# Kernel optimization log

Measured on AMD Instinct MI355X. Metric: run time of the kernel, lower is better.

## Reference

```python
import jax, jax.numpy as jnp
import numpy as np

D_MODEL = 1024
NUM_HEADS = 16
MODULUS = 2147483647
B, S = 2, 2048


def setup_inputs() -> dict:
    key = jax.random.key(0)
    d = D_MODEL
    names_dims = [
        ('q_w', d, d), ('k_w', d, d), ('v_w', d, d), ('o_w', d, d),
        ('emb1_w', 1, d // 2), ('emb2_w', d // 2, d),
        ('log_w', 1, d // 4), ('prime_w', 10, d // 4),
        ('div_w', 20, d // 4), ('bit_w', 32, d // 4),
        ('fus_w', d, d),
    ]
    ks = jax.random.split(key, len(names_dims) + 3)
    inp = {}
    for (name, fin, fout), k in zip(names_dims, ks[:len(names_dims)]):
        inp[name] = jax.random.normal(k, (fin, fout), jnp.float32) * 0.02
        inp[name.replace('_w', '_b')] = jnp.zeros((fout,), jnp.float32)
    inp['arith_bias'] = jax.random.normal(ks[-3], (NUM_HEADS, 1, 1), jnp.float32)
    inp['gcd_weight'] = jnp.ones((1,), jnp.float32)
    inp['encodings'] = jax.random.randint(ks[-2], (B, S), 1, 1000000, dtype=jnp.int32)
    return inp


def reference(encodings, q_w, q_b, k_w, k_b, v_w, v_b, o_w, o_b,
              emb1_w, emb1_b, emb2_w, emb2_b, log_w, log_b,
              prime_w, prime_b, div_w, div_b, bit_w, bit_b,
              fus_w, fus_b, arith_bias, gcd_weight):
    Bz, Sz = encodings.shape
    d = q_w.shape[0]
    H = NUM_HEADS
    hd = d // H

    # --- ArithmeticEmbedding ---
    ef = encodings.astype(jnp.float32)
    norm = (ef / MODULUS)[..., None]                       # [B,S,1]
    base = jnp.maximum(norm @ emb1_w + emb1_b, 0.0) @ emb2_w + emb2_b
    logf = jnp.log(ef + 1.0)[..., None] @ log_w + log_b    # [B,S,d/4]
    primes = jnp.array([2, 3, 5, 7, 11, 13, 17, 19, 23, 29], dtype=jnp.int32)
    pf = (encodings[..., None] % primes == 0).astype(jnp.float32) @ prime_w + prime_b
    tv = jnp.arange(2, 22, dtype=jnp.int32)
    df = ((encodings[..., None] % tv).astype(jnp.float32) / tv.astype(jnp.float32)) @ div_w + div_b
    shifts = jnp.arange(32, dtype=jnp.int32)
    bf = (((encodings[..., None] >> shifts) & 1)).astype(jnp.float32) @ bit_w + bit_b
    feats = jnp.concatenate([logf, pf, df, bf], axis=-1)   # [B,S,d]
    hidden = base + feats @ fus_w + fus_b

    # --- ArithmeticAttention ---
    q = (hidden @ q_w + q_b).reshape(Bz, Sz, H, hd)
    k = (hidden @ k_w + k_b).reshape(Bz, Sz, H, hd)
    v = (hidden @ v_w + v_b).reshape(Bz, Sz, H, hd)
    scores = jnp.einsum('bihd,bjhd->bhij', q, k) / jnp.sqrt(jnp.float32(hd))
    # vectorized arithmetic bias (original is an O(S^2) python loop)
    ei = encodings[:, :, None]
    ej = encodings[:, None, :]
    gcd_approx = jnp.minimum(ei % (ej + 1), ej % (ei + 1)).astype(jnp.float32)
    bias = gcd_approx / (jnp.maximum(ei, ej) + 1).astype(jnp.float32)
    bias = jnp.where(jnp.eye(Sz, dtype=bool)[None], 0.0, bias)  # i==j -> 0
    scores = scores + bias[:, None] * gcd_weight + arith_bias
    attn = jax.nn.softmax(scores, axis=-1)
    out = jnp.einsum('bhij,bjhd->bihd', attn, v).reshape(Bz, Sz, d)
    return out @ o_w + o_b
```

## Files before the change

### kernel.cpp

```cpp
#include <hip/hip_runtime.h>
#include <hip/hip_bf16.h>

typedef unsigned short u16;
typedef __attribute__((ext_vector_type(8))) __bf16 bf16x8;
typedef __attribute__((ext_vector_type(4))) float f32x4;
typedef __attribute__((ext_vector_type(16))) float f32x16;

#define SEQ 2048
#define NB 2
#define NH 16
#define HD 64
#define DM 1024
#define LDQKV 3072
#define KF 576
#define LOG2E 1.4426950408889634f
#define NSPL 3

__device__ __forceinline__ u16 f2bf(float f) {
    unsigned u = __float_as_uint(f);
    unsigned r = u + 0x7FFFu + ((u >> 16) & 1u);
    return (u16)(r >> 16);
}
__device__ __forceinline__ float bf2f(u16 x) {
    return __uint_as_float(((unsigned)x) << 16);
}
__device__ __forceinline__ unsigned cvt_pk_bf16(float a, float b) {
    unsigned r;
    asm("v_cvt_pk_bf16_f32 %0, %1, %2" : "=v"(r) : "v"(a), "v"(b));
    return r;
}
__device__ __forceinline__ void gl_lds16(const u16* g, u16* l) {
    __builtin_amdgcn_global_load_lds((const __attribute__((address_space(1))) unsigned int*)g,
                                     (__attribute__((address_space(3))) unsigned int*)l, 16, 0, 0);
}
__device__ __forceinline__ unsigned fmod_u24(unsigned a, unsigned b) {
    float q = truncf(__fdividef((float)a, (float)b));
    int r = (int)a - (int)((unsigned)q * b);
    r += (r < 0) ? (int)b : 0;
    r -= (r >= (int)b) ? (int)b : 0;
    return (unsigned)r;
}

__global__ __launch_bounds__(256) void transw4_kernel(const float* __restrict__ q_w,
                                                      const float* __restrict__ k_w,
                                                      const float* __restrict__ v_w,
                                                      const float* __restrict__ o_w,
                                                      u16* __restrict__ WqkvT,
                                                      u16* __restrict__ WoT) {
    __shared__ float tl[32][33];
    const int z = blockIdx.z;
    const float* src = (z == 0) ? q_w : (z == 1) ? k_w : (z == 2) ? v_w : o_w;
    u16* dst = (z < 3) ? WqkvT + (size_t)z * 1024 * DM : WoT;
    const float scale = (z == 0) ? 0.125f * LOG2E : 1.0f;
    int tx = threadIdx.x, ty = threadIdx.y;
    int n = blockIdx.x * 32 + tx;
    int kbase = blockIdx.y * 32;
#pragma unroll
    for (int i = 0; i < 4; ++i)
        tl[ty + i * 8][tx] = src[(size_t)(kbase + ty + i * 8) * DM + n];
    __syncthreads();
    int k = kbase + tx;
#pragma unroll
    for (int i = 0; i < 4; ++i) {
        int n2 = blockIdx.x * 32 + ty + i * 8;
        dst[(size_t)n2 * DM + k] = f2bf(tl[tx][ty + i * 8] * scale);
    }
}

__global__ __launch_bounds__(256) void castwc_kernel(const float* __restrict__ src,
                                                     u16* __restrict__ Wc) {
    int i = (blockIdx.x * 256 + threadIdx.x) * 4;
    float4 v = *(const float4*)&src[i];
    uint2 o;
    o.x = cvt_pk_bf16(v.x, v.y);
    o.y = cvt_pk_bf16(v.z, v.w);
    *(uint2*)&Wc[i] = o;
}

__global__ void cvec_kernel(const float* __restrict__ emb2_b, const float* __restrict__ fus_b,
                            const float* __restrict__ log_b, const float* __restrict__ prime_b,
                            const float* __restrict__ div_b, const float* __restrict__ bit_b,
                            const float* __restrict__ fus_w, float* __restrict__ cvec) {
    int n = blockIdx.x * 256 + threadIdx.x;
    float acc = emb2_b[n] + fus_b[n];
#pragma unroll 4
    for (int m = 0; m < 256; ++m) {
        acc += log_b[m]   * fus_w[(size_t)m * DM + n];
        acc += prime_b[m] * fus_w[(size_t)(256 + m) * DM + n];
        acc += div_b[m]   * fus_w[(size_t)(512 + m) * DM + n];
        acc += bit_b[m]   * fus_w[(size_t)(768 + m) * DM + n];
    }
    cvec[n] = acc;
}

__global__ __launch_bounds__(256) void fold_kernel(const float* __restrict__ log_w,
                                                   const float* __restrict__ prime_w,
                                                   const float* __restrict__ div_w,
                                                   const float* __restrict__ bit_w,
                                                   const float* __restrict__ fus_w,
                                                   const float* __restrict__ cvec,
                                                   u16* __restrict__ Wc) {
    const int r = blockIdx.y;
    const int n = blockIdx.x * 256 + threadIdx.x;
    if (r == 63) { Wc[(size_t)575 * DM + n] = f2bf(cvec[n]); return; }
    const float* wrow; int chunk;
    if (r == 0)       { wrow = log_w;                 chunk = 0;   }
    else if (r < 11)  { wrow = prime_w + (r - 1) * 256; chunk = 256; }
    else if (r < 31)  { wrow = div_w + (r - 11) * 256;  chunk = 512; }
    else              { wrow = bit_w + (r - 31) * 256;  chunk = 768; }
    float acc = 0.f;
#pragma unroll 8
    for (int m = 0; m < 256; ++m)
        acc += wrow[m] * fus_w[(size_t)(chunk + m) * DM + n];
    Wc[(size_t)(512 + r) * DM + n] = f2bf(acc);
}

__global__ void qkvb_kernel(const float* __restrict__ q_b, const float* __restrict__ k_b,
                            const float* __restrict__ v_b, float* __restrict__ qkvb) {
    int i = blockIdx.x * 256 + threadIdx.x;
    const float C1 = 0.125f * LOG2E;
    qkvb[i] = (i < 1024) ? q_b[i] * C1 : (i < 2048 ? k_b[i - 1024] : v_b[i - 2048]);
}

__global__ __launch_bounds__(256) void feat_kernel(const int* __restrict__ enc,
                                                   const float* __restrict__ emb1_w,
                                                   const float* __restrict__ emb1_b,
                                                   u16* __restrict__ F) {
    const int tok = blockIdx.x;
    const int t = threadIdx.x;
    int e = enc[tok];
    float ef = (float)e;
    float nrm = ef / 2147483647.0f;
    for (int k = t; k < 512; k += 256)
        F[(size_t)tok * KF + k] = f2bf(fmaxf(nrm * emb1_w[k] + emb1_b[k], 0.f));
    if (t < 64) {
        float v;
        if (t == 0) v = logf(ef + 1.f);
        else if (t < 11) {
            const int pr[10] = {2, 3, 5, 7, 11, 13, 17, 19, 23, 29};
            v = (e % pr[t - 1] == 0) ? 1.f : 0.f;
        } else if (t < 31) {
            int tv = t - 11 + 2;
            v = (float)(e % tv) / (float)tv;
        } else if (t < 63) {
            int sh = t - 31;
            v = (float)((e >> sh) & 1);
        } else v = 1.0f;
        F[(size_t)tok * KF + 512 + t] = f2bf(v);
    }
}

template <int OUT_BF16, int TN, int HB>
__global__ __launch_bounds__(256) void gemm_kernel(const u16* __restrict__ A,
                                                   const u16* __restrict__ BT,
                                                   const float* __restrict__ bias,
                                                   void* __restrict__ Cv,
                                                   int M, int N, int K) {
    constexpr int FN = TN / 32;
    __shared__ u16 As[128 * 32];
    __shared__ u16 Bs[TN * 32];
    const int t = threadIdx.x;
    const int w = t >> 6, l = t & 63, lr = l & 15, lg = l >> 4;
    const int m0 = blockIdx.y * 128, n0 = blockIdx.x * TN;
    const int wm = (w >> 1) * 64, wn = (w & 1) * (TN / 2);
    const int srow = l >> 2, scol = (l & 3) * 8;

    const u16* gA = &A[(size_t)(m0 + w * 32 + srow) * K + scol];
    u16* lA = &As[w * 1024];
    const u16* gB;
    u16* lB;
    if (TN == 128) { gB = &BT[(size_t)(n0 + w * 32 + srow) * K + scol]; lB = &Bs[w * 1024]; }
    else           { gB = &BT[(size_t)(n0 + w * 16 + srow) * K + scol]; lB = &Bs[w * 512];  }

    f32x4 acc[4][FN] = {};
    for (int k0 = 0; k0 < K; k0 += 32) {
        __syncthreads();
        gl_lds16(gA + k0, lA);
        gl_lds16(gA + k0 + (size_t)16 * K, lA + 512);
        if (TN == 128) {
            gl_lds16(gB + k0, lB);
            gl_lds16(gB + k0 + (size_t)16 * K, lB + 512);
        } else {
            gl_lds16(gB + k0, lB);
        }
        __syncthreads();
        bf16x8 a[4], b[FN];
#pragma unroll
        for (int i = 0; i < 4; ++i) a[i] = *(const bf16x8*)&As[(wm + i * 16 + lr) * 32 + lg * 8];
#pragma unroll
        for (int j = 0; j < FN; ++j) b[j] = *(const bf16x8*)&Bs[(wn + j * 16 + lr) * 32 + lg * 8];
#pragma unroll
        for (int mi = 0; mi < 4; ++mi)
#pragma unroll
            for (int ni = 0; ni < FN; ++ni)
                acc[mi][ni] = __builtin_amdgcn_mfma_f32_16x16x32_bf16(a[mi], b[ni], acc[mi][ni], 0, 0, 0);
    }
#pragma unroll
    for (int mi = 0; mi < 4; ++mi)
#pragma unroll
        for (int ni = 0; ni < FN; ++ni)
#pragma unroll
            for (int r = 0; r < 4; ++r) {
                int row = m0 + wm + mi * 16 + lg * 4 + r;
                int col = n0 + wn + ni * 16 + lr;
                float v = acc[mi][ni][r] + (HB ? bias[col] : 0.f);
                if (OUT_BF16)
                    ((u16*)Cv)[(size_t)row * N + col] = f2bf(v);
                else
                    ((float*)Cv)[(size_t)row * N + col] = v;
            }
}

__global__ __launch_bounds__(256) void vtrans_kernel(const u16* __restrict__ qkv,
                                                     u16* __restrict__ vT) {
    __shared__ u16 tile[64][72];
    int t = threadIdx.x;
    int s0 = blockIdx.x * 64, h = blockIdx.y, b = blockIdx.z;
    int sr = t >> 2, sc = (t & 3) * 16;
    const int4* g = (const int4*)&qkv[(size_t)(b * SEQ + s0 + sr) * LDQKV + 2048 + h * HD + sc];
    int4 v0 = g[0], v1 = g[1];
    *(int4*)&tile[sr][sc] = v0;
    *(int4*)&tile[sr][sc + 8] = v1;
    __syncthreads();
    int dl = sr, j0 = sc;
    u16 tmp[16];
#pragma unroll
    for (int jj = 0; jj < 16; ++jj) tmp[jj] = tile[j0 + jj][dl];
    u16* out = &vT[(size_t)((b * NH + h) * HD + dl) * SEQ + s0 + j0];
    *(int4*)&out[0] = *(int4*)&tmp[0];
    *(int4*)&out[8] = *(int4*)&tmp[8];
}

__global__ __launch_bounds__(256) void biasm_kernel(const int* __restrict__ enc,
                                                    const float* __restrict__ gcd_w,
                                                    float* __restrict__ bias2) {
    int vi = blockIdx.x * 256 + threadIdx.x;
    int i  = vi & 2047;
    int rr = (vi >> 11) & 15;
    int jt = (vi >> 15) & 31;
    int b  = vi >> 20;
    int j0 = jt * 64 + rr * 4;
    unsigned ei = (unsigned)enc[b * SEQ + i];
    float scale = gcd_w[0] * LOG2E;
    f32x4 o;
#pragma unroll
    for (int e = 0; e < 4; ++e) {
        int j = j0 + e;
        unsigned ej = (unsigned)enc[b * SEQ + j];
        unsigned r1 = fmod_u24(ei, ej + 1u);
        unsigned r2 = fmod_u24(ej, ei + 1u);
        float g = (float)min(r1, r2);
        float mx = (float)(max(ei, ej) + 1u);
        o[e] = (i == j) ? 0.f : __fdividef(g, mx) * scale;
    }
    *(f32x4*)&bias2[(size_t)vi * 4] = o;
}

#define KVB 64
#define SWZ(row, cb) ((((int)(row)) << 7) + (((int)(cb)) ^ ((((int)(row)) & 7) << 4)))

__global__ __launch_bounds__(256, 3) void attn_kernel(const u16* __restrict__ qkv,
                                                      const u16* __restrict__ vT,
                                                      const float* __restrict__ bias2,
                                                      u16* __restrict__ Opart,
                                                      float* __restrict__ Lp,
                                                      float* __restrict__ Mp) {
    __shared__ char smem[49152];
    const int t = threadIdx.x, w = t >> 6, l = t & 63;
    const int q5 = l & 31, hi = l >> 5;
    char* PlB = smem + 32768 + (w << 12);
    const int qt = blockIdx.x, h = blockIdx.y;
    const int b = blockIdx.z / NSPL, sp = blockIdx.z % NSPL;
    const int qrow = qt * 128 + w * 32 + q5;
    const int jt0 = sp * 11;
    const int NT  = (sp == 2) ? 10 : 11;
    const int j0s = jt0 * KVB;

    bf16x8 qf[4];
#pragma unroll
    for (int ks = 0; ks < 4; ++ks)
        qf[ks] = *(const bf16x8*)&qkv[(size_t)(b * SEQ + qrow) * LDQKV + h * HD + ks * 16 + hi * 8];

    const int sr = t >> 2, sc = (t & 3) * 16;
    const u16* gK = &qkv[(size_t)(b * SEQ + j0s + sr) * LDQKV + 1024 + h * HD + sc];
    const u16* gV = &vT[(size_t)((b * NH + h) * HD + sr) * SEQ + j0s + sc];
    const float* gBl = &bias2[((((size_t)b * 32 + jt0) * 16 + hi) * 2048 + qrow) * 4];

    int4 kr0 = *(const int4*)&gK[0], kr1 = *(const int4*)&gK[8];
    int4 vr0 = *(const int4*)&gV[0], vr1 = *(const int4*)&gV[8];
    f32x4 br[8];
#pragma unroll
    for (int c = 0; c < 2; ++c)
#pragma unroll
        for (int g = 0; g < 4; ++g)
            br[c * 4 + g] = *(const f32x4*)&gBl[(size_t)(8 * c + 2 * g) << 13];

    float m_s = -1e30f, l_s = 0.f;
    f32x16 acc2[2] = {};

    for (int lt = 0; lt < NT; ++lt) {
        char* KtB = smem + (lt & 1) * 16384;
        char* VtB = KtB + 8192;
        *(int4*)(KtB + SWZ(sr, (t & 3) * 32))      = kr0;
        *(int4*)(KtB + SWZ(sr, (t & 3) * 32 + 16)) = kr1;
        *(int4*)(VtB + SWZ(sr, (t & 3) * 32))      = vr0;
        *(int4*)(VtB + SWZ(sr, (t & 3) * 32 + 16)) = vr1;
        if (lt < NT - 1) {
            kr0 = *(const int4*)&gK[(size_t)(lt + 1) * KVB * LDQKV];
            kr1 = *(const int4*)&gK[(size_t)(lt + 1) * KVB * LDQKV + 8];
            vr0 = *(const int4*)&gV[(lt + 1) * KVB];
            vr1 = *(const int4*)&gV[(lt + 1) * KVB + 8];
        }
        __syncthreads();

        f32x16 s2[2];
#pragma unroll
        for (int c = 0; c < 2; ++c)
#pragma unroll
            for (int g = 0; g < 4; ++g)
#pragma unroll
                for (int e = 0; e < 4; ++e)
                    s2[c][g * 4 + e] = br[c * 4 + g][e];
        if (lt < NT - 1) {
            const float* nB = gBl + ((size_t)(lt + 1) << 17);
#pragma unroll
            for (int c = 0; c < 2; ++c)
#pragma unroll
                for (int g = 0; g < 4; ++g)
                    br[c * 4 + g] = *(const f32x4*)&nB[(size_t)(8 * c + 2 * g) << 13];
        }

        __builtin_amdgcn_s_setprio(1);
#pragma unroll
        for (int ks = 0; ks < 4; ++ks)
#pragma unroll
            for (int c = 0; c < 2; ++c) {
                bf16x8 kf = *(const bf16x8*)(KtB + SWZ(32 * c + q5, ks * 32 + hi * 16));
                s2[c] = __builtin_amdgcn_mfma_f32_32x32x16_bf16(kf, qf[ks], s2[c], 0, 0, 0);
            }
        __builtin_amdgcn_s_setprio(0);

        float tm = s2[0][0];
#pragma unroll
        for (int c = 0; c < 2; ++c)
#pragma unroll
            for (int r = 0; r < 16; ++r) tm = fmaxf(tm, s2[c][r]);
        tm = fmaxf(tm, __shfl_xor(tm, 32));

        if (__any(tm > m_s + 8.f)) {
            float mn = fmaxf(m_s, tm);
            float al = __builtin_exp2f(m_s - mn);
            l_s *= al;
            m_s = mn;
#pragma unroll
            for (int dc = 0; dc < 2; ++dc)
#pragma unroll
                for (int r = 0; r < 16; ++r) acc2[dc][r] *= al;
        }

        float ps = 0.f;
#pragma unroll
        for (int c = 0; c < 2; ++c)
#pragma unroll
            for (int r = 0; r < 16; ++r) {
                float p = __builtin_exp2f(s2[c][r] - m_s);
                s2[c][r] = p;
                ps += p;
            }
        ps += __shfl_xor(ps, 32);
        l_s += ps;

#pragma unroll
        for (int c = 0; c < 2; ++c)
#pragma unroll
            for (int g = 0; g < 4; ++g) {
                uint2 u;
                u.x = cvt_pk_bf16(s2[c][4 * g + 0], s2[c][4 * g + 1]);
                u.y = cvt_pk_bf16(s2[c][4 * g + 2], s2[c][4 * g + 3]);
                *(uint2*)(PlB + SWZ(q5, (32 * c + 8 * g + 4 * hi) * 2)) = u;
            }
        asm volatile("s_waitcnt lgkmcnt(0)" ::: "memory");
        __builtin_amdgcn_sched_barrier(0);

        __builtin_amdgcn_s_setprio(1);
#pragma unroll
        for (int ks = 0; ks < 4; ++ks) {
            bf16x8 pb = *(const bf16x8*)(PlB + SWZ(q5, ks * 32 + hi * 16));
#pragma unroll
            for (int dc = 0; dc < 2; ++dc) {
                bf16x8 vf = *(const bf16x8*)(VtB + SWZ(32 * dc + q5, ks * 32 + hi * 16));
                acc2[dc] = __builtin_amdgcn_mfma_f32_32x32x16_bf16(vf, pb, acc2[dc], 0, 0, 0);
            }
        }
        __builtin_amdgcn_s_setprio(0);
    }

    u16* orow = &Opart[(size_t)((sp * NB + b) * SEQ + qrow) * DM + h * HD];
#pragma unroll
    for (int dc = 0; dc < 2; ++dc)
#pragma unroll
        for (int g = 0; g < 4; ++g) {
            uint2 u;
            u.x = cvt_pk_bf16(acc2[dc][4 * g + 0], acc2[dc][4 * g + 1]);
            u.y = cvt_pk_bf16(acc2[dc][4 * g + 2], acc2[dc][4 * g + 3]);
            *(uint2*)&orow[32 * dc + 8 * g + 4 * hi] = u;
        }
    if (hi == 0) {
        size_t idx = ((size_t)(sp * NB + b) * SEQ + qrow) * NH + h;
        Lp[idx] = l_s;
        Mp[idx] = m_s;
    }
}

__global__ __launch_bounds__(256) void comb_kernel(const u16* __restrict__ Opart,
                                                   const float* __restrict__ Lp,
                                                   const float* __restrict__ Mp,
                                                   u16* __restrict__ attn_o) {
    int tid = blockIdx.x * 256 + threadIdx.x;
    int base = tid * 4;
    int b = base / (SEQ * DM);
    int rem = base - b * SEQ * DM;
    int i = rem / DM;
    int c = rem - i * DM;
    int h = c >> 6;
    size_t ix[3];
    float m[3], lv[3];
#pragma unroll
    for (int s = 0; s < 3; ++s) {
        ix[s] = ((size_t)(s * NB + b) * SEQ + i) * NH + h;
        m[s] = Mp[ix[s]];
        lv[s] = Lp[ix[s]];
    }
    float ms = fmaxf(fmaxf(m[0], m[1]), m[2]);
    float a0 = __builtin_exp2f(m[0] - ms);
    float a1 = __builtin_exp2f(m[1] - ms);
    float a2 = __builtin_exp2f(m[2] - ms);
    float inv = 1.f / (a0 * lv[0] + a1 * lv[1] + a2 * lv[2]);
    a0 *= inv; a1 *= inv; a2 *= inv;
    uint2 o0 = *(const uint2*)&Opart[((size_t)(0 * NB + b) * SEQ + i) * DM + c];
    uint2 o1 = *(const uint2*)&Opart[((size_t)(1 * NB + b) * SEQ + i) * DM + c];
    uint2 o2 = *(const uint2*)&Opart[((size_t)(2 * NB + b) * SEQ + i) * DM + c];
    float v0 = a0 * bf2f(o0.x & 0xFFFF) + a1 * bf2f(o1.x & 0xFFFF) + a2 * bf2f(o2.x & 0xFFFF);
    float v1 = a0 * bf2f(o0.x >> 16)    + a1 * bf2f(o1.x >> 16)    + a2 * bf2f(o2.x >> 16);
    float v2 = a0 * bf2f(o0.y & 0xFFFF) + a1 * bf2f(o1.y & 0xFFFF) + a2 * bf2f(o2.y & 0xFFFF);
    float v3 = a0 * bf2f(o0.y >> 16)    + a1 * bf2f(o1.y >> 16)    + a2 * bf2f(o2.y >> 16);
    uint2 u;
    u.x = cvt_pk_bf16(v0, v1);
    u.y = cvt_pk_bf16(v2, v3);
    *(uint2*)&attn_o[(size_t)(b * SEQ + i) * DM + c] = u;
}

extern "C" void kernel_launch(void* const* d_in, const int* in_sizes, int n_in,
                              void* d_out, int out_size, void* d_ws, size_t ws_size,
                              hipStream_t stream) {
    const float* q_w    = (const float*)d_in[0];
    const float* q_b    = (const float*)d_in[1];
    const float* k_w    = (const float*)d_in[2];
    const float* k_b    = (const float*)d_in[3];
    const float* v_w    = (const float*)d_in[4];
    const float* v_b    = (const float*)d_in[5];
    const float* o_w    = (const float*)d_in[6];
    const float* o_b    = (const float*)d_in[7];
    const float* emb1_w = (const float*)d_in[8];
    const float* emb1_b = (const float*)d_in[9];
    const float* emb2_w = (const float*)d_in[10];
    const float* emb2_b = (const float*)d_in[11];
    const float* log_w  = (const float*)d_in[12];
    const float* log_b  = (const float*)d_in[13];
    const float* prime_w= (const float*)d_in[14];
    const float* prime_b= (const float*)d_in[15];
    const float* div_w  = (const float*)d_in[16];
    const float* div_b  = (const float*)d_in[17];
    const float* bit_w  = (const float*)d_in[18];
    const float* bit_b  = (const float*)d_in[19];
    const float* fus_w  = (const float*)d_in[20];
    const float* fus_b  = (const float*)d_in[21];
    const float* gcd_weight = (const float*)d_in[23];
    const int*   enc    = (const int*)d_in[24];

    char* ws = (char*)d_ws;
    size_t off = 0;
    auto alloc = [&](size_t bytes) {
        char* p = ws + off;
        off += (bytes + 255) & ~size_t(255);
        return p;
    };
    u16*   WqkvT  = (u16*)alloc((size_t)3072 * DM * 2);
    u16*   WoT    = (u16*)alloc((size_t)DM * DM * 2);
    u16*   Wc     = (u16*)alloc((size_t)KF * DM * 2);
    u16*   W2T    = (u16*)alloc((size_t)3072 * KF * 2);
    float* cvec   = (float*)alloc(DM * 4);
    float* qkvb   = (float*)alloc(3072 * 4);
    u16*   F      = (u16*)alloc((size_t)NB * SEQ * KF * 2);
    u16*   qkv    = (u16*)alloc((size_t)NB * SEQ * LDQKV * 2);
    u16*   vT     = (u16*)alloc((size_t)NB * NH * HD * SEQ * 2);
    float* bias2  = (float*)alloc((size_t)NB * SEQ * SEQ * 4);
    u16*   attn_o = (u16*)alloc((size_t)NB * SEQ * DM * 2);
    u16*   Opart  = (u16*)alloc((size_t)NSPL * NB * SEQ * DM * 2);
    float* Lp     = (float*)alloc((size_t)NSPL * NB * SEQ * NH * 4);
    float* Mp     = (float*)alloc((size_t)NSPL * NB * SEQ * NH * 4);
    (void)ws_size; (void)n_in; (void)in_sizes; (void)out_size;

    transw4_kernel<<<dim3(32, 32, 4), dim3(32, 8), 0, stream>>>(q_w, k_w, v_w, o_w, WqkvT, WoT);
    castwc_kernel<<<512, 256, 0, stream>>>(emb2_w, Wc);
    cvec_kernel<<<4, 256, 0, stream>>>(emb2_b, fus_b, log_b, prime_b, div_b, bit_b, fus_w, cvec);
    fold_kernel<<<dim3(4, 64), 256, 0, stream>>>(log_w, prime_w, div_w, bit_w, fus_w, cvec, Wc);
    qkvb_kernel<<<12, 256, 0, stream>>>(q_b, k_b, v_b, qkvb);

    gemm_kernel<1, 64, 0><<<dim3(KF / 64, 3072 / 128), 256, 0, stream>>>(WqkvT, Wc, nullptr, W2T,
                                                                         3072, KF, DM);
    feat_kernel<<<NB * SEQ, 256, 0, stream>>>(enc, emb1_w, emb1_b, F);
    gemm_kernel<1, 128, 1><<<dim3(3072 / 128, NB * SEQ / 128), 256, 0, stream>>>(F, W2T, qkvb, qkv,
                                                                                 NB * SEQ, 3072, KF);
    vtrans_kernel<<<dim3(SEQ / 64, NH, NB), 256, 0, stream>>>(qkv, vT);
    biasm_kernel<<<NB * 32 * 16 * SEQ / 256, 256, 0, stream>>>(enc, gcd_weight, bias2);
    attn_kernel<<<dim3(SEQ / 128, NH, NB * NSPL), 256, 0, stream>>>(qkv, vT, bias2, Opart, Lp, Mp);
    comb_kernel<<<NB * SEQ * DM / 4 / 256, 256, 0, stream>>>(Opart, Lp, Mp, attn_o);
    gemm_kernel<0, 64, 1><<<dim3(DM / 64, NB * SEQ / 128), 256, 0, stream>>>(attn_o, WoT, o_b, d_out,
                                                                             NB * SEQ, DM, DM);
}
```

Before: 225.3 us.

## Merge prep kernels and feed bias tile directly as MFMA accumulator

Several small setup kernels (weight cast, cvec, qkv bias, features, bias matrix) are folded into fewer launches: the emb2 cast joins the transpose kernel, cvec moves into fold_kernel, and the bias, feature and qkv-bias work are combined into one prep kernel. The arithmetic bias is rewritten in an MFMA-accumulator-native layout so the attention kernel loads it as two 16-float vectors and passes it as the initial accumulator of the first QK MFMA, removing the per-element register shuffle. This cuts launch overhead and attention register moves, at the cost of a more intricate index mapping that must match the MFMA output layout exactly.

```diff
diff --git a/kernel.cpp b/kernel.cpp
--- a/kernel.cpp
+++ b/kernel.cpp
@@ -41,18 +41,31 @@
     return (unsigned)r;
 }
 
-__global__ __launch_bounds__(256) void transw4_kernel(const float* __restrict__ q_w,
+__global__ __launch_bounds__(256) void transw5_kernel(const float* __restrict__ q_w,
                                                       const float* __restrict__ k_w,
                                                       const float* __restrict__ v_w,
                                                       const float* __restrict__ o_w,
+                                                      const float* __restrict__ emb2_w,
                                                       u16* __restrict__ WqkvT,
-                                                      u16* __restrict__ WoT) {
+                                                      u16* __restrict__ WoT,
+                                                      u16* __restrict__ Wc) {
+    const int z = blockIdx.z;
+    int tx = threadIdx.x, ty = threadIdx.y;
+    if (z >= 4) {
+        int blin = blockIdx.y * 32 + blockIdx.x;
+        if (blin >= 512) return;
+        int i = (blin * 256 + ty * 32 + tx) * 4;
+        float4 v = *(const float4*)&emb2_w[i];
+        uint2 o;
+        o.x = cvt_pk_bf16(v.x, v.y);
+        o.y = cvt_pk_bf16(v.z, v.w);
+        *(uint2*)&Wc[i] = o;
+        return;
+    }
     __shared__ float tl[32][33];
-    const int z = blockIdx.z;
     const float* src = (z == 0) ? q_w : (z == 1) ? k_w : (z == 2) ? v_w : o_w;
     u16* dst = (z < 3) ? WqkvT + (size_t)z * 1024 * DM : WoT;
     const float scale = (z == 0) ? 0.125f * LOG2E : 1.0f;
-    int tx = threadIdx.x, ty = threadIdx.y;
     int n = blockIdx.x * 32 + tx;
     int kbase = blockIdx.y * 32;
 #pragma unroll
@@ -65,32 +78,6 @@
         int n2 = blockIdx.x * 32 + ty + i * 8;
         dst[(size_t)n2 * DM + k] = f2bf(tl[tx][ty + i * 8] * scale);
     }
-}
-
-__global__ __launch_bounds__(256) void castwc_kernel(const float* __restrict__ src,
-                                                     u16* __restrict__ Wc) {
-    int i = (blockIdx.x * 256 + threadIdx.x) * 4;
-    float4 v = *(const float4*)&src[i];
-    uint2 o;
-    o.x = cvt_pk_bf16(v.x, v.y);
-    o.y = cvt_pk_bf16(v.z, v.w);
-    *(uint2*)&Wc[i] = o;
-}
-
-__global__ void cvec_kernel(const float* __restrict__ emb2_b, const float* __restrict__ fus_b,
-                            const float* __restrict__ log_b, const float* __restrict__ prime_b,
-                            const float* __restrict__ div_b, const float* __restrict__ bit_b,
-                            const float* __restrict__ fus_w, float* __restrict__ cvec) {
-    int n = blockIdx.x * 256 + threadIdx.x;
-    float acc = emb2_b[n] + fus_b[n];
-#pragma unroll 4
-    for (int m = 0; m < 256; ++m) {
-        acc += log_b[m]   * fus_w[(size_t)m * DM + n];
-        acc += prime_b[m] * fus_w[(size_t)(256 + m) * DM + n];
-        acc += div_b[m]   * fus_w[(size_t)(512 + m) * DM + n];
-        acc += bit_b[m]   * fus_w[(size_t)(768 + m) * DM + n];
-    }
-    cvec[n] = acc;
 }
 
 __global__ __launch_bounds__(256) void fold_kernel(const float* __restrict__ log_w,
@@ -98,11 +85,27 @@
                                                    const float* __restrict__ div_w,
                                                    const float* __restrict__ bit_w,
                                                    const float* __restrict__ fus_w,
-                                                   const float* __restrict__ cvec,
+                                                   const float* __restrict__ emb2_b,
+                                                   const float* __restrict__ fus_b,
+                                                   const float* __restrict__ log_b,
+                                                   const float* __restrict__ prime_b,
+                                                   const float* __restrict__ div_b,
+                                                   const float* __restrict__ bit_b,
                                                    u16* __restrict__ Wc) {
     const int r = blockIdx.y;
     const int n = blockIdx.x * 256 + threadIdx.x;
-    if (r == 63) { Wc[(size_t)575 * DM + n] = f2bf(cvec[n]); return; }
+    if (r == 63) {
+        float acc = emb2_b[n] + fus_b[n];
+#pragma unroll 4
+        for (int m = 0; m < 256; ++m) {
+            acc += log_b[m]   * fus_w[(size_t)m * DM + n];
+            acc += prime_b[m] * fus_w[(size_t)(256 + m) * DM + n];
+            acc += div_b[m]   * fus_w[(size_t)(512 + m) * DM + n];
+            acc += bit_b[m]   * fus_w[(size_t)(768 + m) * DM + n];
+        }
+        Wc[(size_t)575 * DM + n] = f2bf(acc);
+        return;
+    }
     const float* wrow; int chunk;
     if (r == 0)       { wrow = log_w;                 chunk = 0;   }
     else if (r < 11)  { wrow = prime_w + (r - 1) * 256; chunk = 256; }
@@ -115,38 +118,62 @@
     Wc[(size_t)(512 + r) * DM + n] = f2bf(acc);
 }
 
-__global__ void qkvb_kernel(const float* __restrict__ q_b, const float* __restrict__ k_b,
-                            const float* __restrict__ v_b, float* __restrict__ qkvb) {
-    int i = blockIdx.x * 256 + threadIdx.x;
-    const float C1 = 0.125f * LOG2E;
-    qkvb[i] = (i < 1024) ? q_b[i] * C1 : (i < 2048 ? k_b[i - 1024] : v_b[i - 2048]);
-}
-
-__global__ __launch_bounds__(256) void feat_kernel(const int* __restrict__ enc,
+__global__ __launch_bounds__(256) void prep_kernel(const int* __restrict__ enc,
+                                                   const float* __restrict__ gcd_w,
                                                    const float* __restrict__ emb1_w,
                                                    const float* __restrict__ emb1_b,
-                                                   u16* __restrict__ F) {
-    const int tok = blockIdx.x;
-    const int t = threadIdx.x;
-    int e = enc[tok];
-    float ef = (float)e;
-    float nrm = ef / 2147483647.0f;
-    for (int k = t; k < 512; k += 256)
-        F[(size_t)tok * KF + k] = f2bf(fmaxf(nrm * emb1_w[k] + emb1_b[k], 0.f));
-    if (t < 64) {
-        float v;
-        if (t == 0) v = logf(ef + 1.f);
-        else if (t < 11) {
-            const int pr[10] = {2, 3, 5, 7, 11, 13, 17, 19, 23, 29};
-            v = (e % pr[t - 1] == 0) ? 1.f : 0.f;
-        } else if (t < 31) {
-            int tv = t - 11 + 2;
-            v = (float)(e % tv) / (float)tv;
-        } else if (t < 63) {
-            int sh = t - 31;
-            v = (float)((e >> sh) & 1);
-        } else v = 1.0f;
-        F[(size_t)tok * KF + 512 + t] = f2bf(v);
+                                                   const float* __restrict__ q_b,
+                                                   const float* __restrict__ k_b,
+                                                   const float* __restrict__ v_b,
+                                                   float* __restrict__ bias3,
+                                                   u16* __restrict__ F,
+                                                   float* __restrict__ qkvb) {
+    const int bx = blockIdx.x, t = threadIdx.x;
+    if (bx < 8192) {
+        int tid = bx * 256 + t;
+        int g = tid & 3, hi = (tid >> 2) & 1, i = (tid >> 3) & 2047, tile2 = tid >> 14;
+        int c = tile2 & 1, jt = (tile2 >> 1) & 31, b = tile2 >> 6;
+        unsigned ei = (unsigned)enc[b * SEQ + i];
+        float scale = gcd_w[0] * LOG2E;
+        int j0 = jt * 64 + 32 * c + 8 * g + 4 * hi;
+        int4 ej4 = *(const int4*)&enc[b * SEQ + j0];
+        f32x4 o;
+#pragma unroll
+        for (int e = 0; e < 4; ++e) {
+            unsigned ej = (unsigned)((e == 0) ? ej4.x : (e == 1) ? ej4.y : (e == 2) ? ej4.z : ej4.w);
+            unsigned r1 = fmod_u24(ei, ej + 1u);
+            unsigned r2 = fmod_u24(ej, ei + 1u);
+            float gg = (float)min(r1, r2);
+            float mx = (float)(max(ei, ej) + 1u);
+            o[e] = (i == j0 + e) ? 0.f : __fdividef(gg, mx) * scale;
+        }
+        *(f32x4*)&bias3[(size_t)tid * 4] = o;
+    } else if (bx < 12288) {
+        const int tok = bx - 8192;
+        int e = enc[tok];
+        float ef = (float)e;
+        float nrm = ef / 2147483647.0f;
+        for (int k = t; k < 512; k += 256)
+            F[(size_t)tok * KF + k] = f2bf(fmaxf(nrm * emb1_w[k] + emb1_b[k], 0.f));
+        if (t < 64) {
+            float v;
+            if (t == 0) v = logf(ef + 1.f);
+            else if (t < 11) {
+                const int pr[10] = {2, 3, 5, 7, 11, 13, 17, 19, 23, 29};
+                v = (e % pr[t - 1] == 0) ? 1.f : 0.f;
+            } else if (t < 31) {
+                int tv = t - 11 + 2;
+                v = (float)(e % tv) / (float)tv;
+            } else if (t < 63) {
+                int sh = t - 31;
+                v = (float)((e >> sh) & 1);
+            } else v = 1.0f;
+            F[(size_t)tok * KF + 512 + t] = f2bf(v);
+        }
+    } else {
+        int i = (bx - 12288) * 256 + t;
+        const float C1 = 0.125f * LOG2E;
+        qkvb[i] = (i < 1024) ? q_b[i] * C1 : (i < 2048 ? k_b[i - 1024] : v_b[i - 2048]);
     }
 }
 
@@ -231,37 +258,12 @@
     *(int4*)&out[8] = *(int4*)&tmp[8];
 }
 
-__global__ __launch_bounds__(256) void biasm_kernel(const int* __restrict__ enc,
-                                                    const float* __restrict__ gcd_w,
-                                                    float* __restrict__ bias2) {
-    int vi = blockIdx.x * 256 + threadIdx.x;
-    int i  = vi & 2047;
-    int rr = (vi >> 11) & 15;
-    int jt = (vi >> 15) & 31;
-    int b  = vi >> 20;
-    int j0 = jt * 64 + rr * 4;
-    unsigned ei = (unsigned)enc[b * SEQ + i];
-    float scale = gcd_w[0] * LOG2E;
-    f32x4 o;
-#pragma unroll
-    for (int e = 0; e < 4; ++e) {
-        int j = j0 + e;
-        unsigned ej = (unsigned)enc[b * SEQ + j];
-        unsigned r1 = fmod_u24(ei, ej + 1u);
-        unsigned r2 = fmod_u24(ej, ei + 1u);
-        float g = (float)min(r1, r2);
-        float mx = (float)(max(ei, ej) + 1u);
-        o[e] = (i == j) ? 0.f : __fdividef(g, mx) * scale;
-    }
-    *(f32x4*)&bias2[(size_t)vi * 4] = o;
-}
-
 #define KVB 64
 #define SWZ(row, cb) ((((int)(row)) << 7) + (((int)(cb)) ^ ((((int)(row)) & 7) << 4)))
 
 __global__ __launch_bounds__(256, 3) void attn_kernel(const u16* __restrict__ qkv,
                                                       const u16* __restrict__ vT,
-                                                      const float* __restrict__ bias2,
+                                                      const float* __restrict__ bias3,
                                                       u16* __restrict__ Opart,
                                                       float* __restrict__ Lp,
                                                       float* __restrict__ Mp) {
@@ -284,16 +286,13 @@
     const int sr = t >> 2, sc = (t & 3) * 16;
     const u16* gK = &qkv[(size_t)(b * SEQ + j0s + sr) * LDQKV + 1024 + h * HD + sc];
     const u16* gV = &vT[(size_t)((b * NH + h) * HD + sr) * SEQ + j0s + sc];
-    const float* gBl = &bias2[((((size_t)b * 32 + jt0) * 16 + hi) * 2048 + qrow) * 4];
+    const float* gB3 = &bias3[((((size_t)(b * 32 + jt0) * 2) * 2048 + qrow) * 2 + hi) * 16];
 
     int4 kr0 = *(const int4*)&gK[0], kr1 = *(const int4*)&gK[8];
     int4 vr0 = *(const int4*)&gV[0], vr1 = *(const int4*)&gV[8];
-    f32x4 br[8];
-#pragma unroll
-    for (int c = 0; c < 2; ++c)
-#pragma unroll
-        for (int g = 0; g < 4; ++g)
-            br[c * 4 + g] = *(const f32x4*)&gBl[(size_t)(8 * c + 2 * g) << 13];
+    f32x16 brv[2];
+    brv[0] = *(const f32x16*)(gB3);
+    brv[1] = *(const f32x16*)(gB3 + 65536);
 
     float m_s = -1e30f, l_s = 0.f;
     f32x16 acc2[2] = {};
@@ -314,25 +313,22 @@
         __syncthreads();
 
         f32x16 s2[2];
-#pragma unroll
-        for (int c = 0; c < 2; ++c)
-#pragma unroll
-            for (int g = 0; g < 4; ++g)
-#pragma unroll
-                for (int e = 0; e < 4; ++e)
-                    s2[c][g * 4 + e] = br[c * 4 + g][e];
+        __builtin_amdgcn_s_setprio(1);
+        {
+            bf16x8 kf0 = *(const bf16x8*)(KtB + SWZ(q5, hi * 16));
+            s2[0] = __builtin_amdgcn_mfma_f32_32x32x16_bf16(kf0, qf[0], brv[0], 0, 0, 0);
+            bf16x8 kf1 = *(const bf16x8*)(KtB + SWZ(32 + q5, hi * 16));
+            s2[1] = __builtin_amdgcn_mfma_f32_32x32x16_bf16(kf1, qf[0], brv[1], 0, 0, 0);
+        }
+        __builtin_amdgcn_s_setprio(0);
         if (lt < NT - 1) {
-            const float* nB = gBl + ((size_t)(lt + 1) << 17);
-#pragma unroll
-            for (int c = 0; c < 2; ++c)
-#pragma unroll
-                for (int g = 0; g < 4; ++g)
-                    br[c * 4 + g] = *(const f32x4*)&nB[(size_t)(8 * c + 2 * g) << 13];
-        }
-
+            const float* nB = gB3 + (size_t)(lt + 1) * 131072;
+            brv[0] = *(const f32x16*)(nB);
+            brv[1] = *(const f32x16*)(nB + 65536);
+        }
         __builtin_amdgcn_s_setprio(1);
 #pragma unroll
-        for (int ks = 0; ks < 4; ++ks)
+        for (int ks = 1; ks < 4; ++ks)
 #pragma unroll
             for (int c = 0; c < 2; ++c) {
                 bf16x8 kf = *(const bf16x8*)(KtB + SWZ(32 * c + q5, ks * 32 + hi * 16));
@@ -489,32 +485,29 @@
     u16*   WoT    = (u16*)alloc((size_t)DM * DM * 2);
     u16*   Wc     = (u16*)alloc((size_t)KF * DM * 2);
     u16*   W2T    = (u16*)alloc((size_t)3072 * KF * 2);
-    float* cvec   = (float*)alloc(DM * 4);
     float* qkvb   = (float*)alloc(3072 * 4);
     u16*   F      = (u16*)alloc((size_t)NB * SEQ * KF * 2);
     u16*   qkv    = (u16*)alloc((size_t)NB * SEQ * LDQKV * 2);
     u16*   vT     = (u16*)alloc((size_t)NB * NH * HD * SEQ * 2);
-    float* bias2  = (float*)alloc((size_t)NB * SEQ * SEQ * 4);
+    float* bias3  = (float*)alloc((size_t)NB * SEQ * SEQ * 4);
     u16*   attn_o = (u16*)alloc((size_t)NB * SEQ * DM * 2);
     u16*   Opart  = (u16*)alloc((size_t)NSPL * NB * SEQ * DM * 2);
     float* Lp     = (float*)alloc((size_t)NSPL * NB * SEQ * NH * 4);
     float* Mp     = (float*)alloc((size_t)NSPL * NB * SEQ * NH * 4);
     (void)ws_size; (void)n_in; (void)in_sizes; (void)out_size;
 
-    transw4_kernel<<<dim3(32, 32, 4), dim3(32, 8), 0, stream>>>(q_w, k_w, v_w, o_w, WqkvT, WoT);
-    castwc_kernel<<<512, 256, 0, stream>>>(emb2_w, Wc);
-    cvec_kernel<<<4, 256, 0, stream>>>(emb2_b, fus_b, log_b, prime_b, div_b, bit_b, fus_w, cvec);
-    fold_kernel<<<dim3(4, 64), 256, 0, stream>>>(log_w, prime_w, div_w, bit_w, fus_w, cvec, Wc);
-    qkvb_kernel<<<12, 256, 0, stream>>>(q_b, k_b, v_b, qkvb);
-
+    transw5_kernel<<<dim3(32, 32, 5), dim3(32, 8), 0, stream>>>(q_w, k_w, v_w, o_w, emb2_w,
+                                                                WqkvT, WoT, Wc);
+    fold_kernel<<<dim3(4, 64), 256, 0, stream>>>(log_w, prime_w, div_w, bit_w, fus_w,
+                                                 emb2_b, fus_b, log_b, prime_b, div_b, bit_b, Wc);
+    prep_kernel<<<12300, 256, 0, stream>>>(enc, gcd_weight, emb1_w, emb1_b, q_b, k_b, v_b,
+                                           bias3, F, qkvb);
     gemm_kernel<1, 64, 0><<<dim3(KF / 64, 3072 / 128), 256, 0, stream>>>(WqkvT, Wc, nullptr, W2T,
                                                                          3072, KF, DM);
-    feat_kernel<<<NB * SEQ, 256, 0, stream>>>(enc, emb1_w, emb1_b, F);
     gemm_kernel<1, 128, 1><<<dim3(3072 / 128, NB * SEQ / 128), 256, 0, stream>>>(F, W2T, qkvb, qkv,
                                                                                  NB * SEQ, 3072, KF);
     vtrans_kernel<<<dim3(SEQ / 64, NH, NB), 256, 0, stream>>>(qkv, vT);
-    biasm_kernel<<<NB * 32 * 16 * SEQ / 256, 256, 0, stream>>>(enc, gcd_weight, bias2);
-    attn_kernel<<<dim3(SEQ / 128, NH, NB * NSPL), 256, 0, stream>>>(qkv, vT, bias2, Opart, Lp, Mp);
+    attn_kernel<<<dim3(SEQ / 128, NH, NB * NSPL), 256, 0, stream>>>(qkv, vT, bias3, Opart, Lp, Mp);
     comb_kernel<<<NB * SEQ * DM / 4 / 256, 256, 0, stream>>>(Opart, Lp, Mp, attn_o);
     gemm_kernel<0, 64, 1><<<dim3(DM / 64, NB * SEQ / 128), 256, 0, stream>>>(attn_o, WoT, o_b, d_out,
                                                                              NB * SEQ, DM, DM);
```

Result: no change. 223.3 us (-0.9%).
